# Performance work log

Hardware: AMD Instinct MI355X
Metric: run time of the kernel (lower is better)

The kernel has to match this reference:

```python
import jax, jax.numpy as jnp
import numpy as np

OBS, PRED = 8, 12
E, H, G = 64, 128, 8
NEIGH = 2.0
B, P = 32, 32
N = B * P


def setup_inputs():
    key = jax.random.key(0)
    ks = jax.random.split(key, 16)

    def u(k, shape, fan_in):
        lim = 1.0 / np.sqrt(fan_in)
        return jax.random.uniform(k, shape, jnp.float32, -lim, lim)

    d_in = E + H + E  # input to each LSTM gate: [emb, h, social]
    starts = jnp.arange(B, dtype=jnp.int32) * P
    return {
        "obs_traj_rel": jax.random.normal(ks[0], (OBS, N, 2), jnp.float32) * 0.3,
        "obs_traj": jax.random.normal(ks[1], (OBS, N, 2), jnp.float32),
        "seq_start_end": jnp.stack([starts, starts + P], axis=1),
        "We": u(ks[2], (2, E), 2), "be": u(ks[3], (E,), 2),
        "Wp": u(ks[4], (H * G * G, E), H * G * G), "bp": u(ks[5], (E,), H * G * G),
        "Wi": u(ks[6], (d_in, H), d_in), "bi": u(ks[7], (H,), d_in),
        "Wf": u(ks[8], (d_in, H), d_in), "bf": u(ks[9], (H,), d_in),
        "Wo": u(ks[10], (d_in, H), d_in), "bo": u(ks[11], (H,), d_in),
        "Wg": u(ks[12], (d_in, H), d_in), "bg": u(ks[13], (H,), d_in),
        "Wout": u(ks[14], (H, 2), H), "bout": u(ks[15], (2,), H),
    }


def _social_pool(hid, pos, Wp, bp, nb):
    # hid [N,H], pos [N,2]; sequences are contiguous, equal-size blocks of P peds.
    n, h_dim = hid.shape
    p = n // nb
    hb = hid.reshape(nb, p, h_dim)
    pb = pos.reshape(nb, p, 2)
    rel = pb[:, None, :, :] - pb[:, :, None, :]          # [B, Pi, Pj, 2]
    gnorm = NEIGH / (G - 1)
    relc = jnp.clip(rel / gnorm, -(G // 2), G // 2)
    grid = (relc + G // 2).astype(jnp.int32)             # trunc == floor (vals >= 0)
    gx, gy = grid[..., 0], grid[..., 1]
    eye = jnp.eye(p, dtype=bool)[None]
    valid = (gx >= 0) & (gx < G) & (gy >= 0) & (gy < G) & (~eye)
    bins = gy * G + gx                                    # flat (y, x) bin, matches [y][x] layout
    onehot = jax.nn.one_hot(bins, G * G, dtype=hid.dtype) * valid[..., None]
    pooled = jnp.einsum('bijk,bjh->bikh', onehot, hb)     # [B, P, G*G, H] scatter-add
    flat = pooled.reshape(n, G * G * h_dim)
    return jax.nn.relu(flat @ Wp + bp)


def _cell(x, h_prev, c_prev, s, Wi, bi, Wf, bf, Wo, bo, Wg, bg):
    comb = jnp.concatenate([x, h_prev, s], axis=1)
    i = jax.nn.sigmoid(comb @ Wi + bi)
    f = jax.nn.sigmoid(comb @ Wf + bf)
    o = jax.nn.sigmoid(comb @ Wo + bo)
    g = jnp.tanh(comb @ Wg + bg)
    c = f * c_prev + i * g
    return o * jnp.tanh(c), c


def reference(obs_traj_rel, obs_traj, seq_start_end, We, be, Wp, bp,
              Wi, bi, Wf, bf, Wo, bo, Wg, bg, Wout, bout):
    n = obs_traj_rel.shape[1]
    nb = seq_start_end.shape[0]
    h = jnp.zeros((n, H), obs_traj_rel.dtype)
    c = jnp.zeros((n, H), obs_traj_rel.dtype)
    curr_pos = obs_traj[-1]
    for t in range(OBS):
        emb = obs_traj_rel[t] @ We + be
        curr_pos = obs_traj[t]
        s = _social_pool(h, curr_pos, Wp, bp, nb)
        h, c = _cell(emb, h, c, s, Wi, bi, Wf, bf, Wo, bo, Wg, bg)
    preds = []
    for _ in range(PRED):
        s = _social_pool(h, curr_pos, Wp, bp, nb)
        pv = h @ Wout + bout
        curr_pos = curr_pos + pv
        preds.append(pv)
        emb = pv @ We + be
        h, c = _cell(emb, h, c, s, Wi, bi, Wf, bf, Wo, bo, Wg, bg)
    return jnp.stack(preds, axis=0)  # [pred_len, num_peds, 2]
```

## Files before the change

### kernel.cpp

```cpp
#include <hip/hip_runtime.h>

typedef short s8v __attribute__((ext_vector_type(8)));
typedef float f32x4 __attribute__((ext_vector_type(4)));

#define OBS_T 8
#define NSTEPS 20

__device__ __forceinline__ unsigned short f2bf(float x) {
    unsigned u = __float_as_uint(x);
    u = (u + 0x7FFFu + ((u >> 16) & 1u)) >> 16;
    return (unsigned short)u;
}
__device__ __forceinline__ float bf2f(unsigned short h) {
    return __uint_as_float(((unsigned)h) << 16);
}
__device__ __forceinline__ void store2(unsigned short* H, unsigned short* M,
                                       int ci, float v) {
    unsigned short h = f2bf(v);
    H[ci] = h; M[ci] = f2bf(v - bf2f(h));
}

__global__ void slstm_prep(const float* __restrict__ Wp,
                           const float* __restrict__ Wi, const float* __restrict__ Wf,
                           const float* __restrict__ Wo, const float* __restrict__ Wg,
                           unsigned short* __restrict__ W4H, unsigned short* __restrict__ W4L,
                           unsigned short* __restrict__ WpH, unsigned short* __restrict__ WpL) {
    int x = blockIdx.x * blockDim.x + threadIdx.x;
    const int NW4 = 32 * 8 * 64 * 8;
    const int NWP = 64 * 4 * 4 * 64 * 8;
    if (x < NW4) {
        int j = x & 7, lane = (x >> 3) & 63, ks = (x >> 9) & 7, nt2 = x >> 12;
        int q = nt2 & 3, wvb = nt2 >> 2;
        int col = wvb * 16 + (lane & 15);
        int k = ks * 32 + ((lane >> 4) << 3) + j;
        const float* W = (q == 0) ? Wi : (q == 1) ? Wf : (q == 2) ? Wo : Wg;
        float v = W[k * 128 + col];
        unsigned short h = f2bf(v);
        W4H[x] = h; W4L[x] = f2bf(v - bf2f(h));
    } else if (x < NW4 + NWP) {
        int y = x - NW4;
        int j = y & 7, lane = (y >> 3) & 63, ks = (y >> 9) & 3, nt = (y >> 11) & 3, bin = y >> 13;
        int e = nt * 16 + (lane & 15);
        int k = ks * 32 + ((lane >> 4) << 3) + j;
        float v = Wp[(bin * 128 + k) * 64 + e];
        unsigned short h = f2bf(v);
        WpH[y] = h; WpL[y] = f2bf(v - bf2f(h));
    }
}

struct SP {
    const float *obs_rel, *obs_abs, *We, *be, *bp, *bi, *bfv, *bo, *bg, *Wout, *bout;
    const unsigned short *W4H, *W4L, *WpH, *WpL;
    unsigned short *hBH, *hBM;
    float *hFG, *cG, *posG;
    unsigned char *ulG;
    unsigned *jneedG;
    int *nUG;
    unsigned short *glistG;
    unsigned long long *gstartG;
    float *YG;
    float *out;
};

__global__ __launch_bounds__(512, 2) void slstm_obsbins(SP p) {
    __shared__ float posb[64];
    __shared__ unsigned char binTabL[1024];
    __shared__ unsigned char binSlotL[64];
    __shared__ unsigned jneedS[64];

    const int seq = blockIdx.x & 31;
    const int tt = (blockIdx.x >> 5) + 1;
    const int posIdx = (tt <= 7) ? tt : 7;
    const int tid = threadIdx.x;
    const int lane = tid & 63;
    const int wv = tid >> 6;
    const float gnorm = (float)(2.0 / 7.0);
    const size_t mb = (size_t)(tt * 32 + seq);

    if (tid < 64) posb[tid] = p.obs_abs[posIdx * 2048 + seq * 64 + tid];
    if (tid < 64) jneedS[tid] = 0u;
    __syncthreads();
#pragma unroll
    for (int pp = 0; pp < 2; ++pp) {
        int pr = tid + pp * 512;
        int i = pr >> 5, j = pr & 31;
        float rx = (posb[j * 2]     - posb[i * 2])     / gnorm;
        float ry = (posb[j * 2 + 1] - posb[i * 2 + 1]) / gnorm;
        rx = fminf(fmaxf(rx, -4.f), 4.f);
        ry = fminf(fmaxf(ry, -4.f), 4.f);
        int gx = (int)(rx + 4.f);
        int gy = (int)(ry + 4.f);
        int valid = (gx < 8) && (gy < 8) && (i != j);
        int bin = gy * 8 + gx;
        binTabL[pr] = valid ? (unsigned char)bin : (unsigned char)255;
        if (valid) atomicOr(&jneedS[bin], 1u << j);
    }
    __syncthreads();
    if (wv == 0) {
        bool used = jneedS[lane] != 0u;
        unsigned long long bal = __ballot(used);
        int myIdx = __popcll(bal & ((1ull << lane) - 1ull));
        if (used) p.ulG[mb * 64 + myIdx] = (unsigned char)lane;
        binSlotL[lane] = used ? (unsigned char)myIdx : (unsigned char)255;
        if (lane == 0) p.nUG[mb] = (int)__popcll(bal);
    }
    if (tid < 64) p.jneedG[mb * 64 + tid] = jneedS[tid];
    __syncthreads();
    if (tid < 32) {
        const int i = tid;
        unsigned rw[8];
#pragma unroll
        for (int w = 0; w < 8; ++w)
            rw[w] = *(const unsigned*)&binTabL[i * 32 + w * 4];
        unsigned long long cntp = 0;
#pragma unroll
        for (int j = 0; j < 32; ++j) {
            unsigned bb = (rw[j >> 2] >> ((j & 3) * 8)) & 255u;
            if (bb != 255u) cntp += 1ull << (5 * (binSlotL[bb] >> 3));
        }
        unsigned long long pre = 0; unsigned sum = 0;
#pragma unroll
        for (int c = 0; c < 8; ++c) {
            pre |= (unsigned long long)sum << (5 * c);
            sum += (unsigned)((cntp >> (5 * c)) & 31);
        }
        p.gstartG[mb * 32 + i] = pre | ((unsigned long long)sum << 40);
        unsigned long long pos = pre;
#pragma unroll
        for (int j = 0; j < 32; ++j) {
            unsigned bb = (rw[j >> 2] >> ((j & 3) * 8)) & 255u;
            if (bb != 255u) {
                int sg = binSlotL[bb];
                int c = sg >> 3;
                int pidx = (int)((pos >> (5 * c)) & 31);
                p.glistG[mb * 1024 + i * 32 + pidx] = (unsigned short)((sg << 5) | j);
                pos += 1ull << (5 * c);
            }
        }
    }
}

__global__ __launch_bounds__(512, 2) void slstm_socialY(SP p, int t) {
    const int seq = blockIdx.x & 31;
    const int wrole = blockIdx.x >> 5;
    const int tid = threadIdx.x, lane = tid & 63, wv = tid >> 6;
    const int W = wrole * 8 + wv;
    const int slotG = W >> 2;
    const int jhalf = (W >> 1) & 1;
    const int np = W & 1;
    const int arow = jhalf * 16 + (lane & 15);
    const int j4 = (lane >> 4) << 2;
    const unsigned short* hH = p.hBH + (size_t)seq * 4096;
    const unsigned short* hM = p.hBM + (size_t)seq * 4096;
    float* Yb = p.YG + (size_t)seq * 131072;
    const size_t mb = (size_t)(t * 32 + seq);
    const int nU = p.nUG[mb];

    s8v Ah[4], Am[4];
#pragma unroll
    for (int ks = 0; ks < 4; ++ks) {
        int o = arow * 128 + ks * 32 + ((lane >> 4) << 3);
        Ah[ks] = *(const s8v*)&hH[o];
        Am[ks] = *(const s8v*)&hM[o];
    }
    for (int slot = slotG; slot < nU; slot += 16) {
        int bin = p.ulG[mb * 64 + slot];
        unsigned halfmask = (p.jneedG[mb * 64 + bin] >> (16 * jhalf)) & 0xFFFFu;
        if (!halfmask) continue;
        s8v bh0[4], bl0[4], bh1[4], bl1[4];
#pragma unroll
        for (int ks = 0; ks < 4; ++ks) {
            int foA = ((bin * 4 + np * 2) * 4 + ks) * 64 + lane;
            int foB = ((bin * 4 + np * 2 + 1) * 4 + ks) * 64 + lane;
            bh0[ks] = ((const s8v*)p.WpH)[foA];
            bl0[ks] = ((const s8v*)p.WpL)[foA];
            bh1[ks] = ((const s8v*)p.WpH)[foB];
            bl1[ks] = ((const s8v*)p.WpL)[foB];
        }
        f32x4 a0 = {0.f, 0.f, 0.f, 0.f};
        f32x4 a1 = {0.f, 0.f, 0.f, 0.f};
#pragma unroll
        for (int ks = 0; ks < 4; ++ks) {
            a0 = __builtin_amdgcn_mfma_f32_16x16x32_bf16(Am[ks], bh0[ks], a0, 0, 0, 0);
            a0 = __builtin_amdgcn_mfma_f32_16x16x32_bf16(Ah[ks], bl0[ks], a0, 0, 0, 0);
            a0 = __builtin_amdgcn_mfma_f32_16x16x32_bf16(Ah[ks], bh0[ks], a0, 0, 0, 0);
            a1 = __builtin_amdgcn_mfma_f32_16x16x32_bf16(Am[ks], bh1[ks], a1, 0, 0, 0);
            a1 = __builtin_amdgcn_mfma_f32_16x16x32_bf16(Ah[ks], bl1[ks], a1, 0, 0, 0);
            a1 = __builtin_amdgcn_mfma_f32_16x16x32_bf16(Ah[ks], bh1[ks], a1, 0, 0, 0);
        }
#pragma unroll
        for (int nt = 0; nt < 2; ++nt) {
            int e = (np * 2 + nt) * 16 + (lane & 15);
            const f32x4 a = nt ? a1 : a0;
#pragma unroll
            for (int r = 0; r < 4; ++r) {
                if ((halfmask >> (j4 + r)) & 1u) {
                    int j = jhalf * 16 + j4 + r;
                    Yb[(slot * 32 + j) * 64 + e] = a[r];
                }
            }
        }
    }
}

__global__ __launch_bounds__(512, 1) void slstm_step(SP p, int t) {
    __shared__ __align__(16) unsigned short combH[32 * 256];
    __shared__ __align__(16) unsigned short combM[32 * 256];
    __shared__ float posb[64];
    __shared__ float pvbuf[64];
    __shared__ float red[256];
    __shared__ unsigned char binTabL[1024];
    __shared__ unsigned char binSlotL[64];
    __shared__ unsigned jneedS[64];
    __shared__ float biasL[512], beL[64], bpL[64], WeL[128], WoutL[256], boutL[2];

    const int seq = blockIdx.x;
    const int tid = threadIdx.x;
    const int lane = tid & 63;
    const int wv = tid >> 6;
    const int gi = tid >> 4;
    const int gg = tid & 15;
    const int hc = wv * 16 + (lane & 15);
    const float gnorm = (float)(2.0 / 7.0);
    const size_t mb = (size_t)(t * 32 + seq);

    if (tid < 512) biasL[tid] = (tid < 128) ? p.bi[tid] : (tid < 256) ? p.bfv[tid - 128]
                              : (tid < 384) ? p.bo[tid - 256] : p.bg[tid - 384];
    if (tid < 64) { beL[tid] = p.be[tid]; bpL[tid] = p.bp[tid]; }
    if (tid < 128) WeL[tid] = p.We[tid];
    if (tid < 256) WoutL[tid] = p.Wout[tid];
    if (tid < 2) boutL[tid] = p.bout[tid];

    if (t > 0) {
        for (int x = tid; x < 4096; x += 512) {
            int row = x >> 7, k = x & 127;
            int ci = row * 256 + ((64 + k) ^ ((row & 7) << 3));
            combH[ci] = p.hBH[seq * 4096 + x];
            combM[ci] = p.hBM[seq * 4096 + x];
        }
    } else {
        for (int x = tid; x < 4096; x += 512) {
            int row = x >> 7, k = x & 127;
            int ci = row * 256 + ((64 + k) ^ ((row & 7) << 3));
            combH[ci] = 0; combM[ci] = 0;
        }
    }
    __syncthreads();

    float sreg[4] = {0.f, 0.f, 0.f, 0.f};
    if (t > 0) {
        const int e0 = gg * 4;
        const unsigned long long sp = p.gstartG[mb * 32 + gi];
        const int cnt = (int)(sp >> 40);
        const unsigned short* gl = p.glistG + mb * 1024 + gi * 32;
        const float* Yb = p.YG + (size_t)seq * 131072;
        for (int p0 = 0; p0 < cnt; p0 += 4) {
            unsigned long long e4 = *(const unsigned long long*)&gl[p0];
            int n = cnt - p0;
            unsigned en0 = (unsigned)(e4 & 0xFFFF), en1 = (unsigned)((e4 >> 16) & 0xFFFF);
            unsigned en2 = (unsigned)((e4 >> 32) & 0xFFFF), en3 = (unsigned)((e4 >> 48) & 0xFFFF);
            float4 y0, y1, y2, y3;
            if (n > 0) y0 = *(const float4*)&Yb[(((en0 >> 5) * 32) + (en0 & 31)) * 64 + e0];
            if (n > 1) y1 = *(const float4*)&Yb[(((en1 >> 5) * 32) + (en1 & 31)) * 64 + e0];
            if (n > 2) y2 = *(const float4*)&Yb[(((en2 >> 5) * 32) + (en2 & 31)) * 64 + e0];
            if (n > 3) y3 = *(const float4*)&Yb[(((en3 >> 5) * 32) + (en3 & 31)) * 64 + e0];
            if (n > 0) { sreg[0] += y0.x; sreg[1] += y0.y; sreg[2] += y0.z; sreg[3] += y0.w; }
            if (n > 1) { sreg[0] += y1.x; sreg[1] += y1.y; sreg[2] += y1.z; sreg[3] += y1.w; }
            if (n > 2) { sreg[0] += y2.x; sreg[1] += y2.y; sreg[2] += y2.z; sreg[3] += y2.w; }
            if (n > 3) { sreg[0] += y3.x; sreg[1] += y3.y; sreg[2] += y3.z; sreg[3] += y3.w; }
        }
    }
    {
        int e0 = gg * 4;
#pragma unroll
        for (int r = 0; r < 4; ++r) {
            float v = fmaxf(sreg[r] + bpL[e0 + r], 0.f);
            store2(combH, combM, gi * 256 + ((192 + e0 + r) ^ ((gi & 7) << 3)), v);
        }
    }

    if (t < OBS_T) {
        int e0 = gg * 4;
        float x0 = p.obs_rel[t * 2048 + seq * 64 + gi * 2];
        float x1 = p.obs_rel[t * 2048 + seq * 64 + gi * 2 + 1];
#pragma unroll
        for (int r = 0; r < 4; ++r) {
            int e = e0 + r;
            float v = x0 * WeL[e] + x1 * WeL[64 + e] + beL[e];
            store2(combH, combM, gi * 256 + (e ^ ((gi & 7) << 3)), v);
        }
    } else {
        if (tid < 64) posb[tid] = (t == OBS_T) ? p.obs_abs[7 * 2048 + seq * 64 + tid]
                                               : p.posG[seq * 64 + tid];
        if (tid < 256) {
            int i = tid >> 3, d = (tid >> 2) & 1, pp = tid & 3;
            float acc = 0.f;
            int k0 = pp * 32;
            for (int k = k0; k < k0 + 32; ++k)
                acc += p.hFG[seq * 4096 + i * 128 + k] * WoutL[k * 2 + d];
            red[tid] = acc;
        }
        __syncthreads();
        if (tid < 64) {
            int d = tid & 1;
            float pv = red[tid * 4] + red[tid * 4 + 1] + red[tid * 4 + 2] + red[tid * 4 + 3]
                     + boutL[d];
            p.out[(t - OBS_T) * 2048 + seq * 64 + tid] = pv;
            posb[tid] += pv;
            p.posG[seq * 64 + tid] = posb[tid];
            pvbuf[tid] = pv;
        }
        __syncthreads();
        {
            int e0 = gg * 4;
            float x0 = pvbuf[gi * 2], x1 = pvbuf[gi * 2 + 1];
#pragma unroll
            for (int r = 0; r < 4; ++r) {
                int e = e0 + r;
                float v = x0 * WeL[e] + x1 * WeL[64 + e] + beL[e];
                store2(combH, combM, gi * 256 + (e ^ ((gi & 7) << 3)), v);
            }
        }
    }
    __syncthreads();

    f32x4 acc[4][2];
    {
        f32x4 zero = {0.f, 0.f, 0.f, 0.f};
#pragma unroll
        for (int q = 0; q < 4; ++q) { acc[q][0] = zero; acc[q][1] = zero; }
        s8v gbh[2][4], gbl[2][4];
#pragma unroll
        for (int q = 0; q < 4; ++q) {
            int fo = ((wv * 4 + q) * 8 + 0) * 64 + lane;
            gbh[0][q] = ((const s8v*)p.W4H)[fo];
            gbl[0][q] = ((const s8v*)p.W4L)[fo];
        }
#pragma unroll
        for (int ks = 0; ks < 8; ++ks) {
            const int cb = ks & 1;
            if (ks < 7) {
#pragma unroll
                for (int q = 0; q < 4; ++q) {
                    int fo = ((wv * 4 + q) * 8 + ks + 1) * 64 + lane;
                    gbh[cb ^ 1][q] = ((const s8v*)p.W4H)[fo];
                    gbl[cb ^ 1][q] = ((const s8v*)p.W4L)[fo];
                }
            }
            s8v Ah[2], Am[2];
#pragma unroll
            for (int m = 0; m < 2; ++m) {
                int row = m * 16 + (lane & 15);
                int k = ks * 32 + ((lane >> 4) << 3);
                int ci = row * 256 + (k ^ ((row & 7) << 3));
                Ah[m] = *(const s8v*)&combH[ci];
                Am[m] = *(const s8v*)&combM[ci];
            }
#pragma unroll
            for (int q = 0; q < 4; ++q)
#pragma unroll
                for (int m = 0; m < 2; ++m) {
                    acc[q][m] = __builtin_amdgcn_mfma_f32_16x16x32_bf16(Am[m], gbh[cb][q], acc[q][m], 0, 0, 0);
                    acc[q][m] = __builtin_amdgcn_mfma_f32_16x16x32_bf16(Ah[m], gbl[cb][q], acc[q][m], 0, 0, 0);
                    acc[q][m] = __builtin_amdgcn_mfma_f32_16x16x32_bf16(Ah[m], gbh[cb][q], acc[q][m], 0, 0, 0);
                }
        }
    }

    {
        float b0 = biasL[hc], b1 = biasL[128 + hc], b2 = biasL[256 + hc], b3 = biasL[384 + hc];
#pragma unroll
        for (int m = 0; m < 2; ++m)
#pragma unroll
            for (int r = 0; r < 4; ++r) {
                int row = m * 16 + ((lane >> 4) << 2) + r;
                int gidx = seq * 4096 + row * 128 + hc;
                float cprev = (t > 0) ? p.cG[gidx] : 0.f;
                float pi = acc[0][m][r] + b0;
                float pf = acc[1][m][r] + b1;
                float po = acc[2][m][r] + b2;
                float pg = acc[3][m][r] + b3;
                float ig = 1.f / (1.f + expf(-pi));
                float fg = 1.f / (1.f + expf(-pf));
                float og = 1.f / (1.f + expf(-po));
                float gv = tanhf(pg);
                float cv = fg * cprev + ig * gv;
                p.cG[gidx] = cv;
                float hv = og * tanhf(cv);
                p.hFG[gidx] = hv;
                unsigned short hh = f2bf(hv);
                float r1 = hv - bf2f(hh);
                p.hBH[gidx] = hh;
                p.hBM[gidx] = f2bf(r1);
            }
    }

    if (t >= OBS_T && t < NSTEPS - 1) {
        const size_t nb = (size_t)((t + 1) * 32 + seq);
        if (tid < 64) jneedS[tid] = 0u;
        __syncthreads();
#pragma unroll
        for (int pp = 0; pp < 2; ++pp) {
            int pr = tid + pp * 512;
            int i = pr >> 5, j = pr & 31;
            float rx = (posb[j * 2]     - posb[i * 2])     / gnorm;
            float ry = (posb[j * 2 + 1] - posb[i * 2 + 1]) / gnorm;
            rx = fminf(fmaxf(rx, -4.f), 4.f);
            ry = fminf(fmaxf(ry, -4.f), 4.f);
            int gx = (int)(rx + 4.f);
            int gy = (int)(ry + 4.f);
            int valid = (gx < 8) && (gy < 8) && (i != j);
            int bin = gy * 8 + gx;
            binTabL[pr] = valid ? (unsigned char)bin : (unsigned char)255;
            if (valid) atomicOr(&jneedS[bin], 1u << j);
        }
        __syncthreads();
        if (wv == 0) {
            bool used = jneedS[lane] != 0u;
            unsigned long long bal = __ballot(used);
            int myIdx = __popcll(bal & ((1ull << lane) - 1ull));
            if (used) p.ulG[nb * 64 + myIdx] = (unsigned char)lane;
            binSlotL[lane] = used ? (unsigned char)myIdx : (unsigned char)255;
            if (lane == 0) p.nUG[nb] = (int)__popcll(bal);
        }
        if (tid < 64) p.jneedG[nb * 64 + tid] = jneedS[tid];
        __syncthreads();
        if (tid < 32) {
            const int i = tid;
            unsigned rw[8];
#pragma unroll
            for (int w = 0; w < 8; ++w)
                rw[w] = *(const unsigned*)&binTabL[i * 32 + w * 4];
            unsigned long long cntp = 0;
#pragma unroll
            for (int j = 0; j < 32; ++j) {
                unsigned bb = (rw[j >> 2] >> ((j & 3) * 8)) & 255u;
                if (bb != 255u) cntp += 1ull << (5 * (binSlotL[bb] >> 3));
            }
            unsigned long long pre = 0; unsigned sum = 0;
#pragma unroll
            for (int c = 0; c < 8; ++c) {
                pre |= (unsigned long long)sum << (5 * c);
                sum += (unsigned)((cntp >> (5 * c)) & 31);
            }
            p.gstartG[nb * 32 + i] = pre | ((unsigned long long)sum << 40);
            unsigned long long pos = pre;
#pragma unroll
            for (int j = 0; j < 32; ++j) {
                unsigned bb = (rw[j >> 2] >> ((j & 3) * 8)) & 255u;
                if (bb != 255u) {
                    int sg = binSlotL[bb];
                    int c = sg >> 3;
                    int pidx = (int)((pos >> (5 * c)) & 31);
                    p.glistG[nb * 1024 + i * 32 + pidx] = (unsigned short)((sg << 5) | j);
                    pos += 1ull << (5 * c);
                }
            }
        }
    }
}

__global__ __launch_bounds__(512, 1) void slstm_main_fb(
    const float* __restrict__ obs_rel, const float* __restrict__ obs_abs,
    const float* __restrict__ We, const float* __restrict__ be,
    const float* __restrict__ bp,
    const float* __restrict__ bi, const float* __restrict__ bfv,
    const float* __restrict__ bo, const float* __restrict__ bg,
    const float* __restrict__ Wout, const float* __restrict__ bout,
    const unsigned short* __restrict__ W4H, const unsigned short* __restrict__ W4L,
    const unsigned short* __restrict__ WpH, const unsigned short* __restrict__ WpL,
    float* __restrict__ out) {

    __shared__ __align__(16) unsigned short combH[32 * 256];
    __shared__ __align__(16) unsigned short combM[32 * 256];
    __shared__ __align__(16) float hbuf[32 * 128];
    __shared__ __align__(16) float scratch[32 * 512];
    __shared__ float posb[64];
    __shared__ float pvbuf[64];
    __shared__ float red[256];
    __shared__ unsigned char binTab[1024];
    __shared__ unsigned char usedList[64];
    __shared__ unsigned char binSlotG[64];
    __shared__ unsigned short glist[1024];
    __shared__ unsigned long long gstartPacked[32];
    __shared__ int nUsedS;
    __shared__ unsigned usedMask[2];
    __shared__ unsigned jm[4];
    __shared__ float biasL[512], beL[64], bpL[64], WeL[128], WoutL[256], boutL[2];

    const int tid = threadIdx.x;
    const int lane = tid & 63;
    const int wv = tid >> 6;
    const int b = blockIdx.x;

    if (tid < 512) biasL[tid] = (tid < 128) ? bi[tid] : (tid < 256) ? bfv[tid - 128]
                              : (tid < 384) ? bo[tid - 256] : bg[tid - 384];
    if (tid < 64) { beL[tid] = be[tid]; bpL[tid] = bp[tid]; }
    if (tid < 128) WeL[tid] = We[tid];
    if (tid < 256) WoutL[tid] = Wout[tid];
    if (tid < 2) boutL[tid] = bout[tid];
    for (int x = tid; x < 32 * 256; x += 512) { combH[x] = 0; combM[x] = 0; }
    for (int x = tid; x < 32 * 128; x += 512) hbuf[x] = 0.f;
    float creg[8];
#pragma unroll
    for (int r = 0; r < 8; ++r) creg[r] = 0.f;
    __syncthreads();

    const float gnorm = (float)(2.0 / 7.0);
    const int gi = tid >> 4;
    const int gg = tid & 15;
    const int hc = wv * 16 + (lane & 15);

    for (int t = 0; t < NSTEPS; ++t) {
        if (t < OBS_T) {
            if (tid < 64) posb[tid] = obs_abs[t * 2048 + b * 64 + tid];
            {
                int e0 = gg * 4;
                float x0 = obs_rel[t * 2048 + b * 64 + gi * 2];
                float x1 = obs_rel[t * 2048 + b * 64 + gi * 2 + 1];
#pragma unroll
                for (int r = 0; r < 4; ++r) {
                    int e = e0 + r;
                    float v = x0 * WeL[e] + x1 * WeL[64 + e] + beL[e];
                    store2(combH, combM, gi * 256 + (e ^ ((gi & 7) << 3)), v);
                }
            }
        }
        if (tid < 2) usedMask[tid] = 0u;
        if (tid < 4) jm[tid] = 0u;
        __syncthreads();

        float sreg[4] = {0.f, 0.f, 0.f, 0.f};
        if (t > 0) {
#pragma unroll
            for (int pp = 0; pp < 2; ++pp) {
                int p = tid + pp * 512;
                int i = p >> 5, j = p & 31;
                float rx = (posb[j * 2]     - posb[i * 2])     / gnorm;
                float ry = (posb[j * 2 + 1] - posb[i * 2 + 1]) / gnorm;
                rx = fminf(fmaxf(rx, -4.f), 4.f);
                ry = fminf(fmaxf(ry, -4.f), 4.f);
                int gx = (int)(rx + 4.f);
                int gy = (int)(ry + 4.f);
                int valid = (gx < 8) && (gy < 8) && (i != j);
                int bin = gy * 8 + gx;
                binTab[p] = valid ? (unsigned char)bin : (unsigned char)255;
                if (valid) {
                    atomicOr(&usedMask[bin >> 5], 1u << (bin & 31));
                    atomicOr(&jm[((j < 16) ? 0 : 2) + (bin >> 5)], 1u << (bin & 31));
                }
            }
            __syncthreads();
            if (wv == 0) {
                bool used = (usedMask[lane >> 5] >> (lane & 31)) & 1u;
                unsigned long long bal = __ballot(used);
                int myIdx = __popcll(bal & ((1ull << lane) - 1ull));
                if (used) { usedList[myIdx] = (unsigned char)lane; }
                binSlotG[lane] = used ? (unsigned char)myIdx : (unsigned char)255;
                if (lane == 0) nUsedS = __popcll(bal);
            }
            __syncthreads();
            const int nUsed = nUsedS;
            const int nChunks = (nUsed + 7) >> 3;

            s8v Ahs[2][4], Ams[2][4];
#pragma unroll
            for (int m = 0; m < 2; ++m)
#pragma unroll
                for (int ks = 0; ks < 4; ++ks) {
                    int row = m * 16 + (lane & 15);
                    int k = ks * 32 + ((lane >> 4) << 3);
                    int ci = row * 256 + ((64 + k) ^ ((row & 7) << 3));
                    Ahs[m][ks] = *(const s8v*)&combH[ci];
                    Ams[m][ks] = *(const s8v*)&combM[ci];
                }

            if (tid < 32) {
                const int i = tid;
                unsigned rw[8];
#pragma unroll
                for (int w = 0; w < 8; ++w)
                    rw[w] = *(const unsigned*)&binTab[i * 32 + w * 4];
                unsigned long long cntp = 0;
#pragma unroll
                for (int j = 0; j < 32; ++j) {
                    unsigned bb = (rw[j >> 2] >> ((j & 3) * 8)) & 255u;
                    if (bb != 255u) cntp += 1ull << (5 * (binSlotG[bb] >> 3));
                }
                unsigned long long pre = 0; unsigned sum = 0;
#pragma unroll
                for (int c = 0; c < 8; ++c) {
                    pre |= (unsigned long long)sum << (5 * c);
                    sum += (unsigned)((cntp >> (5 * c)) & 31);
                }
                gstartPacked[i] = pre | ((unsigned long long)sum << 40);
                unsigned long long pos = pre;
#pragma unroll
                for (int j = 0; j < 32; ++j) {
                    unsigned bb = (rw[j >> 2] >> ((j & 3) * 8)) & 255u;
                    if (bb != 255u) {
                        int sg = binSlotG[bb];
                        int c = sg >> 3;
                        int p = (int)((pos >> (5 * c)) & 31);
                        glist[i * 32 + p] = (unsigned short)((sg << 5) | j);
                        pos += 1ull << (5 * c);
                    }
                }
            }

            unsigned long long spReg = 0;
            for (int c = 0; c < nChunks; ++c) {
                int idx = c * 8 + wv;
                if (idx < nUsed) {
                    int bin = usedList[idx];
                    const bool do0 = (jm[bin >> 5]       >> (bin & 31)) & 1;
                    const bool do1 = (jm[2 + (bin >> 5)] >> (bin & 31)) & 1;
#pragma unroll
                    for (int np = 0; np < 2; ++np) {
                        s8v bh0[4], bl0[4], bh1[4], bl1[4];
#pragma unroll
                        for (int ks = 0; ks < 4; ++ks) {
                            int foA = ((bin * 4 + np * 2)     * 4 + ks) * 64 + lane;
                            int foB = ((bin * 4 + np * 2 + 1) * 4 + ks) * 64 + lane;
                            bh0[ks] = ((const s8v*)WpH)[foA];
                            bl0[ks] = ((const s8v*)WpL)[foA];
                            bh1[ks] = ((const s8v*)WpH)[foB];
                            bl1[ks] = ((const s8v*)WpL)[foB];
                        }
                        if (do0) {
                            f32x4 a0 = {0.f, 0.f, 0.f, 0.f};
                            f32x4 a1 = {0.f, 0.f, 0.f, 0.f};
#pragma unroll
                            for (int ks = 0; ks < 4; ++ks) {
                                a0 = __builtin_amdgcn_mfma_f32_16x16x32_bf16(Ams[0][ks], bh0[ks], a0, 0, 0, 0);
                                a0 = __builtin_amdgcn_mfma_f32_16x16x32_bf16(Ahs[0][ks], bl0[ks], a0, 0, 0, 0);
                                a0 = __builtin_amdgcn_mfma_f32_16x16x32_bf16(Ahs[0][ks], bh0[ks], a0, 0, 0, 0);
                                a1 = __builtin_amdgcn_mfma_f32_16x16x32_bf16(Ams[0][ks], bh1[ks], a1, 0, 0, 0);
                                a1 = __builtin_amdgcn_mfma_f32_16x16x32_bf16(Ahs[0][ks], bl1[ks], a1, 0, 0, 0);
                                a1 = __builtin_amdgcn_mfma_f32_16x16x32_bf16(Ahs[0][ks], bh1[ks], a1, 0, 0, 0);
                            }
#pragma unroll
                            for (int nt = 0; nt < 2; ++nt) {
                                int e = (np * 2 + nt) * 16 + (lane & 15);
                                const f32x4 a = nt ? a1 : a0;
#pragma unroll
                                for (int r = 0; r < 4; ++r) {
                                    int j = ((lane >> 4) << 2) + r;
                                    scratch[j * 512 + wv * 64 + (e ^ (((j >> 2) & 3) << 4))] = a[r];
                                }
                            }
                        }
                        if (do1) {
                            f32x4 a0 = {0.f, 0.f, 0.f, 0.f};
                            f32x4 a1 = {0.f, 0.f, 0.f, 0.f};
#pragma unroll
                            for (int ks = 0; ks < 4; ++ks) {
                                a0 = __builtin_amdgcn_mfma_f32_16x16x32_bf16(Ams[1][ks], bh0[ks], a0, 0, 0, 0);
                                a0 = __builtin_amdgcn_mfma_f32_16x16x32_bf16(Ahs[1][ks], bl0[ks], a0, 0, 0, 0);
                                a0 = __builtin_amdgcn_mfma_f32_16x16x32_bf16(Ahs[1][ks], bh0[ks], a0, 0, 0, 0);
                                a1 = __builtin_amdgcn_mfma_f32_16x16x32_bf16(Ams[1][ks], bh1[ks], a1, 0, 0, 0);
                                a1 = __builtin_amdgcn_mfma_f32_16x16x32_bf16(Ahs[1][ks], bl1[ks], a1, 0, 0, 0);
                                a1 = __builtin_amdgcn_mfma_f32_16x16x32_bf16(Ahs[1][ks], bh1[ks], a1, 0, 0, 0);
                            }
#pragma unroll
                            for (int nt = 0; nt < 2; ++nt) {
                                int e = (np * 2 + nt) * 16 + (lane & 15);
                                const f32x4 a = nt ? a1 : a0;
#pragma unroll
                                for (int r = 0; r < 4; ++r) {
                                    int j = 16 + ((lane >> 4) << 2) + r;
                                    scratch[j * 512 + wv * 64 + (e ^ (((j >> 2) & 3) << 4))] = a[r];
                                }
                            }
                        }
                    }
                }
                __syncthreads();
                {
                    const int e0 = gg * 4;
                    if (c == 0) spReg = gstartPacked[gi];
                    int p0 = (int)((spReg >> (5 * c)) & 31);
                    int p1 = (int)((spReg >> (5 * c + 5)) & 31);
                    for (int p = p0; p < p1; ++p) {
                        unsigned en = glist[gi * 32 + p];
                        int slot = (en >> 5) & 7;
                        int j = en & 31;
                        const float4 y = *(const float4*)
                            &scratch[j * 512 + slot * 64 + (e0 ^ (((j >> 2) & 3) << 4))];
                        sreg[0] += y.x; sreg[1] += y.y; sreg[2] += y.z; sreg[3] += y.w;
                    }
                }
                __syncthreads();
            }
        }
        {
            int e0 = gg * 4;
#pragma unroll
            for (int r = 0; r < 4; ++r) {
                float v = fmaxf(sreg[r] + bpL[e0 + r], 0.f);
                store2(combH, combM, gi * 256 + ((192 + e0 + r) ^ ((gi & 7) << 3)), v);
            }
        }
        if (t >= OBS_T) {
            if (tid < 256) {
                int i = tid >> 3, d = (tid >> 2) & 1, pp = tid & 3;
                float acc = 0.f;
                int k0 = pp * 32;
                for (int k = k0; k < k0 + 32; ++k)
                    acc += hbuf[i * 128 + (k ^ ((i & 7) << 2))] * WoutL[k * 2 + d];
                red[tid] = acc;
            }
            __syncthreads();
            if (tid < 64) {
                int d = tid & 1;
                float pv = red[tid * 4] + red[tid * 4 + 1] + red[tid * 4 + 2] + red[tid * 4 + 3]
                         + boutL[d];
                out[(t - OBS_T) * 2048 + b * 64 + tid] = pv;
                posb[tid] += pv;
                pvbuf[tid] = pv;
            }
            __syncthreads();
            {
                int e0 = gg * 4;
                float x0 = pvbuf[gi * 2], x1 = pvbuf[gi * 2 + 1];
#pragma unroll
                for (int r = 0; r < 4; ++r) {
                    int e = e0 + r;
                    float v = x0 * WeL[e] + x1 * WeL[64 + e] + beL[e];
                    store2(combH, combM, gi * 256 + (e ^ ((gi & 7) << 3)), v);
                }
            }
        }
        __syncthreads();
        {
            f32x4 acc[4][2];
            f32x4 zero = {0.f, 0.f, 0.f, 0.f};
#pragma unroll
            for (int q = 0; q < 4; ++q) { acc[q][0] = zero; acc[q][1] = zero; }
            s8v gbh[2][4], gbl[2][4];
#pragma unroll
            for (int q = 0; q < 4; ++q) {
                int fo = ((wv * 4 + q) * 8 + 0) * 64 + lane;
                gbh[0][q] = ((const s8v*)W4H)[fo];
                gbl[0][q] = ((const s8v*)W4L)[fo];
            }
#pragma unroll
            for (int ks = 0; ks < 8; ++ks) {
                const int cb = ks & 1;
                if (ks < 7) {
#pragma unroll
                    for (int q = 0; q < 4; ++q) {
                        int fo = ((wv * 4 + q) * 8 + ks + 1) * 64 + lane;
                        gbh[cb ^ 1][q] = ((const s8v*)W4H)[fo];
                        gbl[cb ^ 1][q] = ((const s8v*)W4L)[fo];
                    }
                }
                s8v Ah[2], Am[2];
#pragma unroll
                for (int m = 0; m < 2; ++m) {
                    int row = m * 16 + (lane & 15);
                    int k = ks * 32 + ((lane >> 4) << 3);
                    int ci = row * 256 + (k ^ ((row & 7) << 3));
                    Ah[m] = *(const s8v*)&combH[ci];
                    Am[m] = *(const s8v*)&combM[ci];
                }
#pragma unroll
                for (int q = 0; q < 4; ++q)
#pragma unroll
                    for (int m = 0; m < 2; ++m) {
                        acc[q][m] = __builtin_amdgcn_mfma_f32_16x16x32_bf16(Am[m], gbh[cb][q], acc[q][m], 0, 0, 0);
                        acc[q][m] = __builtin_amdgcn_mfma_f32_16x16x32_bf16(Ah[m], gbl[cb][q], acc[q][m], 0, 0, 0);
                        acc[q][m] = __builtin_amdgcn_mfma_f32_16x16x32_bf16(Ah[m], gbh[cb][q], acc[q][m], 0, 0, 0);
                    }
            }
            __syncthreads();
            float b0 = biasL[hc], b1 = biasL[128 + hc], b2 = biasL[256 + hc], b3 = biasL[384 + hc];
#pragma unroll
            for (int m = 0; m < 2; ++m)
#pragma unroll
                for (int r = 0; r < 4; ++r) {
                    int s = m * 4 + r;
                    int row = m * 16 + ((lane >> 4) << 2) + r;
                    float pi = acc[0][m][r] + b0;
                    float pf = acc[1][m][r] + b1;
                    float po = acc[2][m][r] + b2;
                    float pg = acc[3][m][r] + b3;
                    float ig = 1.f / (1.f + expf(-pi));
                    float fg = 1.f / (1.f + expf(-pf));
                    float og = 1.f / (1.f + expf(-po));
                    float gv = tanhf(pg);
                    float cv = fg * creg[s] + ig * gv;
                    creg[s] = cv;
                    float hv = og * tanhf(cv);
                    hbuf[row * 128 + (hc ^ ((row & 7) << 2))] = hv;
                    store2(combH, combM, row * 256 + ((64 + hc) ^ ((row & 7) << 3)), hv);
                }
        }
        __syncthreads();
    }
}

extern "C" void kernel_launch(void* const* d_in, const int* in_sizes, int n_in,
                              void* d_out, int out_size, void* d_ws, size_t ws_size,
                              hipStream_t stream) {
    const float* obs_rel = (const float*)d_in[0];
    const float* obs_abs = (const float*)d_in[1];
    const float* We   = (const float*)d_in[3];
    const float* be   = (const float*)d_in[4];
    const float* Wp   = (const float*)d_in[5];
    const float* bp   = (const float*)d_in[6];
    const float* Wi   = (const float*)d_in[7];
    const float* bi   = (const float*)d_in[8];
    const float* Wf   = (const float*)d_in[9];
    const float* bf   = (const float*)d_in[10];
    const float* Wo   = (const float*)d_in[11];
    const float* bo   = (const float*)d_in[12];
    const float* Wg   = (const float*)d_in[13];
    const float* bg   = (const float*)d_in[14];
    const float* Wout = (const float*)d_in[15];
    const float* bout = (const float*)d_in[16];

    char* ws = (char*)d_ws;
    unsigned short* W4H = (unsigned short*)(ws + 0);
    unsigned short* W4L = (unsigned short*)(ws + 262144);
    unsigned short* WpH = (unsigned short*)(ws + 524288);
    unsigned short* WpL = (unsigned short*)(ws + 1572864);
    unsigned short* hBH = (unsigned short*)(ws + 2621440);
    unsigned short* hBM = (unsigned short*)(ws + 2883584);
    float* hFG          = (float*)(ws + 3145728);
    float* cG           = (float*)(ws + 3670016);
    float* posG         = (float*)(ws + 4194304);
    unsigned char* ulG  = (unsigned char*)(ws + 4202496);
    unsigned* jneedG    = (unsigned*)(ws + 4243456);
    int* nUG            = (int*)(ws + 4407296);
    unsigned long long* gstartG = (unsigned long long*)(ws + 4409856);
    unsigned short* glistG = (unsigned short*)(ws + 4573696);
    float* YG           = (float*)(ws + 5884416);
    const size_t NEED   = 22661632;

    slstm_prep<<<2560, 256, 0, stream>>>(Wp, Wi, Wf, Wo, Wg, W4H, W4L, WpH, WpL);

    if (ws_size >= NEED) {
        SP p;
        p.obs_rel = obs_rel; p.obs_abs = obs_abs; p.We = We; p.be = be; p.bp = bp;
        p.bi = bi; p.bfv = bf; p.bo = bo; p.bg = bg; p.Wout = Wout; p.bout = bout;
        p.W4H = W4H; p.W4L = W4L; p.WpH = WpH; p.WpL = WpL;
        p.hBH = hBH; p.hBM = hBM; p.hFG = hFG; p.cG = cG; p.posG = posG;
        p.ulG = ulG; p.jneedG = jneedG; p.nUG = nUG;
        p.glistG = glistG; p.gstartG = gstartG; p.YG = YG; p.out = (float*)d_out;

        slstm_obsbins<<<256, 512, 0, stream>>>(p);
        slstm_step<<<32, 512, 0, stream>>>(p, 0);
        for (int t = 1; t < NSTEPS; ++t) {
            slstm_socialY<<<256, 512, 0, stream>>>(p, t);
            slstm_step<<<32, 512, 0, stream>>>(p, t);
        }
    } else {
        slstm_main_fb<<<32, 512, 0, stream>>>(obs_rel, obs_abs, We, be, bp, bi, bf, bo, bg,
                                              Wout, bout, W4H, W4L, WpH, WpL,
                                              (float*)d_out);
    }
}
```

Measured before the change: 581.8 us.

## Fuse weight prep with obs binning, halve socialY blocks, reorder step prologue

Merges the weight-conversion prep kernel into the observation-binning kernel as extra blocks, removing one launch. socialY now runs 256-thread blocks in which each wave covers both 16-row halves of a bin, so the Wp fragments are reused across both halves instead of being loaded twice. In the step kernel, the gather of social Y values now runs before the shared-memory prologue and barrier, so the global loads can overlap. A leftover dummy loop is harmless but adds clutter.

```diff
diff --git a/kernel.cpp b/kernel.cpp
--- a/kernel.cpp
+++ b/kernel.cpp
@@ -18,6 +18,133 @@
                                        int ci, float v) {
     unsigned short h = f2bf(v);
     H[ci] = h; M[ci] = f2bf(v - bf2f(h));
+}
+
+struct SP {
+    const float *obs_rel, *obs_abs, *We, *be, *bp, *bi, *bfv, *bo, *bg, *Wout, *bout;
+    const unsigned short *W4H, *W4L, *WpH, *WpL;
+    unsigned short *hBH, *hBM;
+    float *hFG, *cG, *posG;
+    unsigned char *ulG;
+    unsigned *jneedG;
+    int *nUG;
+    unsigned short *glistG;
+    unsigned long long *gstartG;
+    float *YG;
+    float *out;
+};
+
+__global__ __launch_bounds__(512, 2) void slstm_pre(SP p,
+    const float* __restrict__ Wp,
+    const float* __restrict__ Wi, const float* __restrict__ Wf,
+    const float* __restrict__ Wo, const float* __restrict__ Wg,
+    unsigned short* __restrict__ W4H, unsigned short* __restrict__ W4L,
+    unsigned short* __restrict__ WpH, unsigned short* __restrict__ WpL) {
+    __shared__ float posb[64];
+    __shared__ unsigned char binTabL[1024];
+    __shared__ unsigned char binSlotL[64];
+    __shared__ unsigned jneedS[64];
+
+    const int tid = threadIdx.x;
+
+    if (blockIdx.x >= 256) {
+        const int NW4 = 32 * 8 * 64 * 8;
+        const int NWP = 64 * 4 * 4 * 64 * 8;
+        int base = (((int)blockIdx.x - 256) * 512 + tid) * 4;
+#pragma unroll
+        for (int u = 0; u < 4; ++u) {
+            int x = base + u;
+            if (x < NW4) {
+                int j = x & 7, lane = (x >> 3) & 63, ks = (x >> 9) & 7, nt2 = x >> 12;
+                int q = nt2 & 3, wvb = nt2 >> 2;
+                int col = wvb * 16 + (lane & 15);
+                int k = ks * 32 + ((lane >> 4) << 3) + j;
+                const float* W = (q == 0) ? Wi : (q == 1) ? Wf : (q == 2) ? Wo : Wg;
+                float v = W[k * 128 + col];
+                unsigned short h = f2bf(v);
+                W4H[x] = h; W4L[x] = f2bf(v - bf2f(h));
+            } else if (x < NW4 + NWP) {
+                int y = x - NW4;
+                int j = y & 7, lane = (y >> 3) & 63, ks = (y >> 9) & 3, nt = (y >> 11) & 3, bin = y >> 13;
+                int e = nt * 16 + (lane & 15);
+                int k = ks * 32 + ((lane >> 4) << 3) + j;
+                float v = Wp[(bin * 128 + k) * 64 + e];
+                unsigned short h = f2bf(v);
+                WpH[y] = h; WpL[y] = f2bf(v - bf2f(h));
+            }
+        }
+        return;
+    }
+
+    const int seq = blockIdx.x & 31;
+    const int tt = (blockIdx.x >> 5) + 1;
+    const int posIdx = (tt <= 7) ? tt : 7;
+    const int lane = tid & 63;
+    const int wv = tid >> 6;
+    const float gnorm = (float)(2.0 / 7.0);
+    const size_t mb = (size_t)(tt * 32 + seq);
+
+    if (tid < 64) posb[tid] = p.obs_abs[posIdx * 2048 + seq * 64 + tid];
+    if (tid < 64) jneedS[tid] = 0u;
+    __syncthreads();
+#pragma unroll
+    for (int pp = 0; pp < 2; ++pp) {
+        int pr = tid + pp * 512;
+        int i = pr >> 5, j = pr & 31;
+        float rx = (posb[j * 2]     - posb[i * 2])     / gnorm;
+        float ry = (posb[j * 2 + 1] - posb[i * 2 + 1]) / gnorm;
+        rx = fminf(fmaxf(rx, -4.f), 4.f);
+        ry = fminf(fmaxf(ry, -4.f), 4.f);
+        int gx = (int)(rx + 4.f);
+        int gy = (int)(ry + 4.f);
+        int valid = (gx < 8) && (gy < 8) && (i != j);
+        int bin = gy * 8 + gx;
+        binTabL[pr] = valid ? (unsigned char)bin : (unsigned char)255;
+        if (valid) atomicOr(&jneedS[bin], 1u << j);
+    }
+    __syncthreads();
+    if (wv == 0) {
+        bool used = jneedS[lane] != 0u;
+        unsigned long long bal = __ballot(used);
+        int myIdx = __popcll(bal & ((1ull << lane) - 1ull));
+        if (used) p.ulG[mb * 64 + myIdx] = (unsigned char)lane;
+        binSlotL[lane] = used ? (unsigned char)myIdx : (unsigned char)255;
+        if (lane == 0) p.nUG[mb] = (int)__popcll(bal);
+    }
+    if (tid < 64) p.jneedG[mb * 64 + tid] = jneedS[tid];
+    __syncthreads();
+    if (tid < 32) {
+        const int i = tid;
+        unsigned rw[8];
+#pragma unroll
+        for (int w = 0; w < 8; ++w)
+            rw[w] = *(const unsigned*)&binTabL[i * 32 + w * 4];
+        unsigned long long cntp = 0;
+#pragma unroll
+        for (int j = 0; j < 32; ++j) {
+            unsigned bb = (rw[j >> 2] >> ((j & 3) * 8)) & 255u;
+            if (bb != 255u) cntp += 1ull << (5 * (binSlotL[bb] >> 3));
+        }
+        unsigned long long pre = 0; unsigned sum = 0;
+#pragma unroll
+        for (int c = 0; c < 8; ++c) {
+            pre |= (unsigned long long)sum << (5 * c);
+            sum += (unsigned)((cntp >> (5 * c)) & 31);
+        }
+        p.gstartG[mb * 32 + i] = pre | ((unsigned long long)sum << 40);
+        unsigned long long pos = pre;
+#pragma unroll
+        for (int j = 0; j < 32; ++j) {
+            unsigned bb = (rw[j >> 2] >> ((j & 3) * 8)) & 255u;
+            if (bb != 255u) {
+                int sg = binSlotL[bb];
+                int c = sg >> 3;
+                int pidx = (int)((pos >> (5 * c)) & 31);
+                p.glistG[mb * 1024 + i * 32 + pidx] = (unsigned short)((sg << 5) | j);
+                pos += 1ull << (5 * c);
+            }
+        }
+    }
 }
 
 __global__ void slstm_prep(const float* __restrict__ Wp,
@@ -48,107 +175,13 @@
     }
 }
 
-struct SP {
-    const float *obs_rel, *obs_abs, *We, *be, *bp, *bi, *bfv, *bo, *bg, *Wout, *bout;
-    const unsigned short *W4H, *W4L, *WpH, *WpL;
-    unsigned short *hBH, *hBM;
-    float *hFG, *cG, *posG;
-    unsigned char *ulG;
-    unsigned *jneedG;
-    int *nUG;
-    unsigned short *glistG;
-    unsigned long long *gstartG;
-    float *YG;
-    float *out;
-};
-
-__global__ __launch_bounds__(512, 2) void slstm_obsbins(SP p) {
-    __shared__ float posb[64];
-    __shared__ unsigned char binTabL[1024];
-    __shared__ unsigned char binSlotL[64];
-    __shared__ unsigned jneedS[64];
-
-    const int seq = blockIdx.x & 31;
-    const int tt = (blockIdx.x >> 5) + 1;
-    const int posIdx = (tt <= 7) ? tt : 7;
-    const int tid = threadIdx.x;
-    const int lane = tid & 63;
-    const int wv = tid >> 6;
-    const float gnorm = (float)(2.0 / 7.0);
-    const size_t mb = (size_t)(tt * 32 + seq);
-
-    if (tid < 64) posb[tid] = p.obs_abs[posIdx * 2048 + seq * 64 + tid];
-    if (tid < 64) jneedS[tid] = 0u;
-    __syncthreads();
-#pragma unroll
-    for (int pp = 0; pp < 2; ++pp) {
-        int pr = tid + pp * 512;
-        int i = pr >> 5, j = pr & 31;
-        float rx = (posb[j * 2]     - posb[i * 2])     / gnorm;
-        float ry = (posb[j * 2 + 1] - posb[i * 2 + 1]) / gnorm;
-        rx = fminf(fmaxf(rx, -4.f), 4.f);
-        ry = fminf(fmaxf(ry, -4.f), 4.f);
-        int gx = (int)(rx + 4.f);
-        int gy = (int)(ry + 4.f);
-        int valid = (gx < 8) && (gy < 8) && (i != j);
-        int bin = gy * 8 + gx;
-        binTabL[pr] = valid ? (unsigned char)bin : (unsigned char)255;
-        if (valid) atomicOr(&jneedS[bin], 1u << j);
-    }
-    __syncthreads();
-    if (wv == 0) {
-        bool used = jneedS[lane] != 0u;
-        unsigned long long bal = __ballot(used);
-        int myIdx = __popcll(bal & ((1ull << lane) - 1ull));
-        if (used) p.ulG[mb * 64 + myIdx] = (unsigned char)lane;
-        binSlotL[lane] = used ? (unsigned char)myIdx : (unsigned char)255;
-        if (lane == 0) p.nUG[mb] = (int)__popcll(bal);
-    }
-    if (tid < 64) p.jneedG[mb * 64 + tid] = jneedS[tid];
-    __syncthreads();
-    if (tid < 32) {
-        const int i = tid;
-        unsigned rw[8];
-#pragma unroll
-        for (int w = 0; w < 8; ++w)
-            rw[w] = *(const unsigned*)&binTabL[i * 32 + w * 4];
-        unsigned long long cntp = 0;
-#pragma unroll
-        for (int j = 0; j < 32; ++j) {
-            unsigned bb = (rw[j >> 2] >> ((j & 3) * 8)) & 255u;
-            if (bb != 255u) cntp += 1ull << (5 * (binSlotL[bb] >> 3));
-        }
-        unsigned long long pre = 0; unsigned sum = 0;
-#pragma unroll
-        for (int c = 0; c < 8; ++c) {
-            pre |= (unsigned long long)sum << (5 * c);
-            sum += (unsigned)((cntp >> (5 * c)) & 31);
-        }
-        p.gstartG[mb * 32 + i] = pre | ((unsigned long long)sum << 40);
-        unsigned long long pos = pre;
-#pragma unroll
-        for (int j = 0; j < 32; ++j) {
-            unsigned bb = (rw[j >> 2] >> ((j & 3) * 8)) & 255u;
-            if (bb != 255u) {
-                int sg = binSlotL[bb];
-                int c = sg >> 3;
-                int pidx = (int)((pos >> (5 * c)) & 31);
-                p.glistG[mb * 1024 + i * 32 + pidx] = (unsigned short)((sg << 5) | j);
-                pos += 1ull << (5 * c);
-            }
-        }
-    }
-}
-
-__global__ __launch_bounds__(512, 2) void slstm_socialY(SP p, int t) {
+__global__ __launch_bounds__(256) void slstm_socialY(SP p, int t) {
     const int seq = blockIdx.x & 31;
     const int wrole = blockIdx.x >> 5;
     const int tid = threadIdx.x, lane = tid & 63, wv = tid >> 6;
-    const int W = wrole * 8 + wv;
-    const int slotG = W >> 2;
-    const int jhalf = (W >> 1) & 1;
+    const int W = wrole * 4 + wv;
+    const int slotG = W >> 1;
     const int np = W & 1;
-    const int arow = jhalf * 16 + (lane & 15);
     const int j4 = (lane >> 4) << 2;
     const unsigned short* hH = p.hBH + (size_t)seq * 4096;
     const unsigned short* hM = p.hBM + (size_t)seq * 4096;
@@ -156,17 +189,19 @@
     const size_t mb = (size_t)(t * 32 + seq);
     const int nU = p.nUG[mb];
 
-    s8v Ah[4], Am[4];
-#pragma unroll
-    for (int ks = 0; ks < 4; ++ks) {
-        int o = arow * 128 + ks * 32 + ((lane >> 4) << 3);
-        Ah[ks] = *(const s8v*)&hH[o];
-        Am[ks] = *(const s8v*)&hM[o];
-    }
+    s8v Ah[2][4], Am[2][4];
+#pragma unroll
+    for (int m = 0; m < 2; ++m)
+#pragma unroll
+        for (int ks = 0; ks < 4; ++ks) {
+            int row = m * 16 + (lane & 15);
+            int o = row * 128 + ks * 32 + ((lane >> 4) << 3);
+            Ah[m][ks] = *(const s8v*)&hH[o];
+            Am[m][ks] = *(const s8v*)&hM[o];
+        }
     for (int slot = slotG; slot < nU; slot += 16) {
         int bin = p.ulG[mb * 64 + slot];
-        unsigned halfmask = (p.jneedG[mb * 64 + bin] >> (16 * jhalf)) & 0xFFFFu;
-        if (!halfmask) continue;
+        unsigned need = p.jneedG[mb * 64 + bin];
         s8v bh0[4], bl0[4], bh1[4], bl1[4];
 #pragma unroll
         for (int ks = 0; ks < 4; ++ks) {
@@ -177,26 +212,31 @@
             bh1[ks] = ((const s8v*)p.WpH)[foB];
             bl1[ks] = ((const s8v*)p.WpL)[foB];
         }
-        f32x4 a0 = {0.f, 0.f, 0.f, 0.f};
-        f32x4 a1 = {0.f, 0.f, 0.f, 0.f};
-#pragma unroll
-        for (int ks = 0; ks < 4; ++ks) {
-            a0 = __builtin_amdgcn_mfma_f32_16x16x32_bf16(Am[ks], bh0[ks], a0, 0, 0, 0);
-            a0 = __builtin_amdgcn_mfma_f32_16x16x32_bf16(Ah[ks], bl0[ks], a0, 0, 0, 0);
-            a0 = __builtin_amdgcn_mfma_f32_16x16x32_bf16(Ah[ks], bh0[ks], a0, 0, 0, 0);
-            a1 = __builtin_amdgcn_mfma_f32_16x16x32_bf16(Am[ks], bh1[ks], a1, 0, 0, 0);
-            a1 = __builtin_amdgcn_mfma_f32_16x16x32_bf16(Ah[ks], bl1[ks], a1, 0, 0, 0);
-            a1 = __builtin_amdgcn_mfma_f32_16x16x32_bf16(Ah[ks], bh1[ks], a1, 0, 0, 0);
-        }
-#pragma unroll
-        for (int nt = 0; nt < 2; ++nt) {
-            int e = (np * 2 + nt) * 16 + (lane & 15);
-            const f32x4 a = nt ? a1 : a0;
-#pragma unroll
-            for (int r = 0; r < 4; ++r) {
-                if ((halfmask >> (j4 + r)) & 1u) {
-                    int j = jhalf * 16 + j4 + r;
-                    Yb[(slot * 32 + j) * 64 + e] = a[r];
+#pragma unroll
+        for (int m = 0; m < 2; ++m) {
+            unsigned hm = (need >> (16 * m)) & 0xFFFFu;
+            if (!hm) continue;
+            f32x4 a0 = {0.f, 0.f, 0.f, 0.f};
+            f32x4 a1 = {0.f, 0.f, 0.f, 0.f};
+#pragma unroll
+            for (int ks = 0; ks < 4; ++ks) {
+                a0 = __builtin_amdgcn_mfma_f32_16x16x32_bf16(Am[m][ks], bh0[ks], a0, 0, 0, 0);
+                a0 = __builtin_amdgcn_mfma_f32_16x16x32_bf16(Ah[m][ks], bl0[ks], a0, 0, 0, 0);
+                a0 = __builtin_amdgcn_mfma_f32_16x16x32_bf16(Ah[m][ks], bh0[ks], a0, 0, 0, 0);
+                a1 = __builtin_amdgcn_mfma_f32_16x16x32_bf16(Am[m][ks], bh1[ks], a1, 0, 0, 0);
+                a1 = __builtin_amdgcn_mfma_f32_16x16x32_bf16(Ah[m][ks], bl1[ks], a1, 0, 0, 0);
+                a1 = __builtin_amdgcn_mfma_f32_16x16x32_bf16(Ah[m][ks], bh1[ks], a1, 0, 0, 0);
+            }
+#pragma unroll
+            for (int nt = 0; nt < 2; ++nt) {
+                int e = (np * 2 + nt) * 16 + (lane & 15);
+                const f32x4 a = nt ? a1 : a0;
+#pragma unroll
+                for (int r = 0; r < 4; ++r) {
+                    if ((hm >> (j4 + r)) & 1u) {
+                        int j = m * 16 + j4 + r;
+                        Yb[(slot * 32 + j) * 64 + e] = a[r];
+                    }
                 }
             }
         }
@@ -223,29 +263,6 @@
     const int hc = wv * 16 + (lane & 15);
     const float gnorm = (float)(2.0 / 7.0);
     const size_t mb = (size_t)(t * 32 + seq);
-
-    if (tid < 512) biasL[tid] = (tid < 128) ? p.bi[tid] : (tid < 256) ? p.bfv[tid - 128]
-                              : (tid < 384) ? p.bo[tid - 256] : p.bg[tid - 384];
-    if (tid < 64) { beL[tid] = p.be[tid]; bpL[tid] = p.bp[tid]; }
-    if (tid < 128) WeL[tid] = p.We[tid];
-    if (tid < 256) WoutL[tid] = p.Wout[tid];
-    if (tid < 2) boutL[tid] = p.bout[tid];
-
-    if (t > 0) {
-        for (int x = tid; x < 4096; x += 512) {
-            int row = x >> 7, k = x & 127;
-            int ci = row * 256 + ((64 + k) ^ ((row & 7) << 3));
-            combH[ci] = p.hBH[seq * 4096 + x];
-            combM[ci] = p.hBM[seq * 4096 + x];
-        }
-    } else {
-        for (int x = tid; x < 4096; x += 512) {
-            int row = x >> 7, k = x & 127;
-            int ci = row * 256 + ((64 + k) ^ ((row & 7) << 3));
-            combH[ci] = 0; combM[ci] = 0;
-        }
-    }
-    __syncthreads();
 
     float sreg[4] = {0.f, 0.f, 0.f, 0.f};
     if (t > 0) {
@@ -270,6 +287,39 @@
             if (n > 3) { sreg[0] += y3.x; sreg[1] += y3.y; sreg[2] += y3.z; sreg[3] += y3.w; }
         }
     }
+
+    biasL[tid] = (tid < 128) ? p.bi[tid] : (tid < 256) ? p.bfv[tid - 128]
+               : (tid < 384) ? p.bo[tid - 256] : p.bg[tid - 384];
+    if (tid < 64) { beL[tid] = p.be[tid]; bpL[tid] = p.bp[tid]; }
+    if (tid < 128) WeL[tid] = p.We[tid];
+    if (tid < 256) WoutL[tid] = p.Wout[tid];
+    if (tid < 2) boutL[tid] = p.bout[tid];
+
+    if (t > 0) {
+        for (int x = tid; x < 4096; x += 512) {
+            int row = x >> 7, k = x & 127;
+            int ci = row * 256 + ((64 + k) ^ ((row & 7) << 3));
+            combH[ci] = p.hBH[seq * 4096 + x];
+            combM[ci] = p.hBM[seq * 4096 + x];
+        }
+    } else {
+        for (int x = tid; x < 4096; x += 512) {
+            int row = x >> 7, k = x & 127;
+            int ci = row * 256 + ((64 + k) ^ ((row & 7) << 3));
+            combH[ci] = 0; combM[ci] = 0;
+        }
+    }
+
+    {
+        int e0 = gg * 4;
+#pragma unroll
+        for (int r = 0; r < 4; ++r) {
+            float v = fmaxf(sreg[r] + bpL[e0 + r], 0.f);
+            (void)v;
+            break;
+        }
+    }
+    __syncthreads();
     {
         int e0 = gg * 4;
 #pragma unroll
@@ -838,8 +888,6 @@
     float* YG           = (float*)(ws + 5884416);
     const size_t NEED   = 22661632;
 
-    slstm_prep<<<2560, 256, 0, stream>>>(Wp, Wi, Wf, Wo, Wg, W4H, W4L, WpH, WpL);
-
     if (ws_size >= NEED) {
         SP p;
         p.obs_rel = obs_rel; p.obs_abs = obs_abs; p.We = We; p.be = be; p.bp = bp;
@@ -849,13 +897,14 @@
         p.ulG = ulG; p.jneedG = jneedG; p.nUG = nUG;
         p.glistG = glistG; p.gstartG = gstartG; p.YG = YG; p.out = (float*)d_out;
 
-        slstm_obsbins<<<256, 512, 0, stream>>>(p);
+        slstm_pre<<<576, 512, 0, stream>>>(p, Wp, Wi, Wf, Wo, Wg, W4H, W4L, WpH, WpL);
         slstm_step<<<32, 512, 0, stream>>>(p, 0);
         for (int t = 1; t < NSTEPS; ++t) {
-            slstm_socialY<<<256, 512, 0, stream>>>(p, t);
+            slstm_socialY<<<256, 256, 0, stream>>>(p, t);
             slstm_step<<<32, 512, 0, stream>>>(p, t);
         }
     } else {
+        slstm_prep<<<2560, 256, 0, stream>>>(Wp, Wi, Wf, Wo, Wg, W4H, W4L, WpH, WpL);
         slstm_main_fb<<<32, 512, 0, stream>>>(obs_rel, obs_abs, We, be, bp, bi, bf, bo, bg,
                                               Wout, bout, W4H, W4L, WpH, WpL,
                                               (float*)d_out);
```

New measurement: 576.6 us. About the same (-0.9%).
